# Kernel tuning notes

Hardware: AMD Instinct MI355X
Metric: run time of the kernel (lower is better)

## Reference

```python
import jax, jax.numpy as jnp
import numpy as np
from jax import lax

C = 173            # EEG channels (independent towers)
L = 400            # samples per channel
POOL_OUT = 10      # AdaptiveMaxPool1d output length (400/10 = 40 exact window)
EPS = 1e-5


def setup_inputs() -> dict:
    key = jax.random.key(0)
    ks = jax.random.split(key, 6)
    B = 64
    x = jax.random.normal(ks[0], (B, C, L), dtype=jnp.float32)
    # per-channel tower 1: Conv1d(1,16,9)  -> grouped kernel [C*16, 1, 9]
    w1 = jax.random.normal(ks[1], (C * 16, 1, 9), dtype=jnp.float32) * 0.2
    b1 = jnp.zeros((C * 16,), jnp.float32)
    g1 = jnp.ones((C * 16,), jnp.float32)
    beta1 = jnp.zeros((C * 16,), jnp.float32)
    m1 = jnp.zeros((C * 16,), jnp.float32)
    v1 = jnp.ones((C * 16,), jnp.float32)
    # per-channel tower 2: Conv1d(16,32,7) -> grouped kernel [C*32, 16, 7]
    w2 = jax.random.normal(ks[2], (C * 32, 16, 7), dtype=jnp.float32) * 0.05
    b2 = jnp.zeros((C * 32,), jnp.float32)
    g2 = jnp.ones((C * 32,), jnp.float32)
    beta2 = jnp.zeros((C * 32,), jnp.float32)
    m2 = jnp.zeros((C * 32,), jnp.float32)
    v2 = jnp.ones((C * 32,), jnp.float32)
    # combiner MLP: Linear(32*C*10, 128) -> ReLU -> Linear(128, 1)
    wc1 = jax.random.normal(ks[3], (128, 32 * C * POOL_OUT), dtype=jnp.float32) * 0.01
    bc1 = jnp.zeros((128,), jnp.float32)
    wc2 = jax.random.normal(ks[4], (1, 128), dtype=jnp.float32) * 0.05
    bc2 = jnp.zeros((1,), jnp.float32)
    return dict(x=x, w1=w1, b1=b1, g1=g1, beta1=beta1, m1=m1, v1=v1,
                w2=w2, b2=b2, g2=g2, beta2=beta2, m2=m2, v2=v2,
                wc1=wc1, bc1=bc1, wc2=wc2, bc2=bc2)


def _bn(y, g, beta, m, v):
    # inference-mode BatchNorm1d over channel axis of [B, CF, L]
    inv = g * lax.rsqrt(v + EPS)
    return y * inv[None, :, None] + (beta - m * inv)[None, :, None]


def reference(x, w1, b1, g1, beta1, m1, v1, w2, b2, g2, beta2, m2, v2, wc1, bc1, wc2, bc2):
    B = x.shape[0]
    dn = ('NCH', 'OIH', 'NCH')
    # tower conv 1: all 173 per-channel Conv1d(1,16,9,pad=4) as one grouped conv
    y = lax.conv_general_dilated(x, w1, (1,), [(4, 4)], dimension_numbers=dn,
                                 feature_group_count=C)           # [B, C*16, 400]
    y = jax.nn.relu(_bn(y + b1[None, :, None], g1, beta1, m1, v1))
    # tower conv 2: Conv1d(16,32,7,pad=3), grouped by channel
    y = lax.conv_general_dilated(y, w2, (1,), [(3, 3)], dimension_numbers=dn,
                                 feature_group_count=C)           # [B, C*32, 400]
    y = jax.nn.relu(_bn(y + b2[None, :, None], g2, beta2, m2, v2))
    # AdaptiveMaxPool1d(10): exact non-overlapping windows of 40
    y = y.reshape(B, C * 32, POOL_OUT, L // POOL_OUT).max(axis=-1)  # [B, C*32, 10]
    # concat of per-channel flattened features == flatten (channel, feat, pos)
    flat = y.reshape(B, C * 32 * POOL_OUT)                          # [B, 55360]
    h = jax.nn.relu(flat @ wc1.T + bc1)
    out = h @ wc2.T + bc2                                           # [B, 1]
    return out
```

## Files before the change

kernel.cpp:

```cpp
#include <hip/hip_runtime.h>

#define C_CH 173
#define L_IN 400
#define EPSV 1e-5f
#define KFEAT 55360

typedef __fp16   fp16x2 __attribute__((ext_vector_type(2)));
typedef _Float16 f16x8  __attribute__((ext_vector_type(8)));
typedef float    f32x4  __attribute__((ext_vector_type(4)));
typedef float    f32x16 __attribute__((ext_vector_type(16)));

#define Y1T_STRIDE_I 9
#define Y1T_ROWS   406

#define SEG_STRIDE 102

#define N1 (173 * 3584)
#define N2 (173 * 512)
#define N3 (173 * 96)

__global__ __launch_bounds__(256) void prep_kernel(
    const float* __restrict__ w1, const float* __restrict__ b1,
    const float* __restrict__ g1, const float* __restrict__ beta1,
    const float* __restrict__ m1, const float* __restrict__ v1,
    const float* __restrict__ w2, const float* __restrict__ b2,
    const float* __restrict__ g2, const float* __restrict__ beta2,
    const float* __restrict__ m2, const float* __restrict__ v2,
    _Float16* __restrict__ w2T_g, _Float16* __restrict__ w1T_g,
    float* __restrict__ sc_g)
{
    const int idx = blockIdx.x * 256 + threadIdx.x;
    if (idx < N1) {
        int c = idx / 3584, r = idx - c * 3584;
        int dt = r >> 9, fg = r & 511;
        int f = fg >> 4, g = fg & 15;
        w2T_g[idx] = (_Float16)w2[c * 3584 + f * 112 + g * 7 + dt];
    } else if (idx < N1 + N2) {
        int j = idx - N1;
        int c = j / 512, r = j - c * 512;
        int g = r >> 5, k = r & 31;
        w1T_g[j] = (k < 9) ? (_Float16)w1[c * 144 + g * 9 + k] : (_Float16)0.0f;
    } else if (idx < N1 + N2 + N3) {
        int j = idx - N1 - N2;
        int c = j / 96, r = j - c * 96;
        float o;
        if (r < 32) {
            int g  = r & 15;
            int cf = c * 16 + g;
            float inv = g1[cf] * rsqrtf(v1[cf] + EPSV);
            o = (r < 16) ? inv : (b1[cf] - m1[cf]) * inv + beta1[cf];
        } else {
            int f  = (r - 32) & 31;
            int cf = c * 32 + f;
            float inv = g2[cf] * rsqrtf(v2[cf] + EPSV);
            o = (r < 64) ? inv : (b2[cf] - m2[cf]) * inv + beta2[cf];
        }
        sc_g[j] = o;
    }
}

__global__ __launch_bounds__(320, 8) void tower_kernel(
    const float* __restrict__ x,
    const _Float16* __restrict__ w2T_g, const _Float16* __restrict__ w1T_g,
    const float* __restrict__ sc_g,
    _Float16* __restrict__ featH)
{
    __shared__ __align__(16) _Float16 xa_s[432];
    __shared__ __align__(16) _Float16 xb_s[432];
    __shared__ __align__(16) _Float16 w1T_s[16 * 32];
    __shared__ __align__(16) _Float16 y1T_s[Y1T_ROWS * 2 * Y1T_STRIDE_I];
    __shared__ __align__(16) _Float16 w2T_s[7 * 512];
    __shared__ _Float16               segmax_s[32 * SEG_STRIDE];
    __shared__ __align__(16) float    cst_s[96];

    const int c   = blockIdx.x;
    const int tid = threadIdx.x;

    {
        const int4* w2src = (const int4*)(w2T_g + (size_t)c * 3584);
        for (int i = tid; i < 448; i += 320) ((int4*)w2T_s)[i] = w2src[i];
        const int4* w1src = (const int4*)(w1T_g + c * 512);
        if (tid < 64) ((int4*)w1T_s)[tid] = w1src[tid];
        const float4* csrc = (const float4*)(sc_g + c * 96);
        if (tid >= 64 && tid < 88) ((float4*)cst_s)[tid - 64] = csrc[tid - 64];
        if (tid >= 88 && tid < 142) {
            int i = tid - 88;
            int r = i / 9, cx = i - r * 9;
            int row = (r < 3) ? r : (400 + r);
            ((int*)y1T_s)[row * Y1T_STRIDE_I + cx] = 0;
        }
    }
    __syncthreads();
    const float s2f  = cst_s[32 + (tid & 31)];
    const float sh2f = cst_s[64 + (tid & 31)];

    for (int nb = 0; nb < 4; ++nb) {
        const int b = blockIdx.y * 4 + nb;

        const float* xrow = x + ((size_t)b * C_CH + c) * L_IN;
        for (int i = tid; i < 432; i += 320) {
            float v = (i >= 4 && i < 404) ? xrow[i - 4] : 0.0f;
            _Float16 h = (_Float16)v;
            xa_s[i] = h;
            if (i > 0) xb_s[i - 1] = h;
        }
        if (tid == 0) xb_s[431] = (_Float16)0.0f;
        __syncthreads();

        {
            const int lane = tid & 63;
            const int wv5  = tid >> 6;
            const int nl   = lane & 15;
            const int q    = lane >> 4;
            union { int4 v; f16x8 h; } a1;
            a1.v = *(const int4*)((const int*)w1T_s + nl * 16 + q * 4);
            float s1r[4], sh1r[4];
#pragma unroll
            for (int r = 0; r < 4; ++r) {
                s1r[r]  = cst_s[q * 4 + r];
                sh1r[r] = cst_s[16 + q * 4 + r];
            }
            const int* xsel = (const int*)((nl & 1) ? xb_s : xa_s);
            for (int tile = 0; tile < 5; ++tile) {
                const int t0 = (wv5 * 5 + tile) * 16;
                const int dw = (t0 + nl + q * 8) >> 1;
                union { int4 v; f16x8 h; } bf;
                bf.v.x = xsel[dw];
                bf.v.y = xsel[dw + 1];
                bf.v.z = xsel[dw + 2];
                bf.v.w = xsel[dw + 3];
                f32x4 acc = {0.0f, 0.0f, 0.0f, 0.0f};
                acc = __builtin_amdgcn_mfma_f32_16x16x32_f16(a1.h, bf.h, acc, 0, 0, 0);
                union { _Float16 h[4]; int2 d; } pk;
#pragma unroll
                for (int r = 0; r < 4; ++r) {
                    float v = acc[r] * s1r[r] + sh1r[r];
                    pk.h[r] = (_Float16)(v > 0.0f ? v : 0.0f);
                }
                int* yp = (int*)y1T_s + (t0 + nl + 3) * Y1T_STRIDE_I + q * 2;
                yp[0] = pk.d.x;
                yp[1] = pk.d.y;
            }
        }
        __syncthreads();

        {
            const int wv    = tid >> 6;
            const int lane  = tid & 63;
            const int nlane = lane & 31;
            const int half  = lane >> 5;

            union F8q { int4 q; f16x8 h; } af[7];
#pragma unroll
            for (int dt = 0; dt < 7; ++dt)
                af[dt].q = *(const int4*)((const int*)w2T_s + dt * 256 + nlane * 8 + half * 4);

            for (int tile = wv; tile < 13; tile += 5) {
                const int tA  = tile * 32 + nlane;
                const int tAr = tA < 400 ? tA : 399;
                f32x16 acc;
#pragma unroll
                for (int i = 0; i < 16; ++i) acc[i] = 0.0f;

#pragma unroll
                for (int dt = 0; dt < 7; ++dt) {
                    const int* p = (const int*)y1T_s + (tAr + dt) * Y1T_STRIDE_I + half * 4;
                    union { int d[4]; f16x8 h; } bf;
                    bf.d[0] = p[0];
                    bf.d[1] = p[1];
                    bf.d[2] = p[2];
                    bf.d[3] = p[3];
                    acc = __builtin_amdgcn_mfma_f32_32x32x16_f16(bf.h, af[dt].h, acc, 0, 0, 0);
                }

                const int base = nlane * SEG_STRIDE + tile * 8 + half;
#pragma unroll
                for (int q = 0; q < 4; ++q) {
                    float v0 = acc[4 * q + 0] * s2f;
                    float v1 = acc[4 * q + 1] * s2f;
                    float v2 = acc[4 * q + 2] * s2f;
                    float v3 = acc[4 * q + 3] * s2f;
                    float m  = fmaxf(fmaxf(v0, v1), fmaxf(v2, v3));
                    const int sub = tile * 8 + 2 * q + half;
                    if (sub < 100) segmax_s[base + 2 * q] = (_Float16)m;
                }
            }
        }
        __syncthreads();

        {
            const int f = tid & 31;
            const int p = tid >> 5;
            float m = -3.0e38f;
#pragma unroll
            for (int k = 0; k < 10; ++k)
                m = fmaxf(m, (float)segmax_s[f * SEG_STRIDE + p * 10 + k]);
            float v = fmaxf(m + sh2f, 0.0f);
            featH[(size_t)b * KFEAT + (c * 32 + f) * 10 + p] = (_Float16)v;
        }
    }
}

__global__ __launch_bounds__(256) void fc1_kernel(
    const _Float16* __restrict__ featH, const float* __restrict__ wc1,
    float* __restrict__ part)
{
    const int tid   = threadIdx.x;
    const int kb    = blockIdx.x;
    const int k0    = kb * 320;
    const int lane  = tid & 63;
    const int wv    = tid >> 6;
    const int nlane = lane & 31;
    const int half  = lane >> 5;
    const int jrow  = wv * 32 + nlane;

    const float*    ap  = wc1   + (size_t)jrow * KFEAT + k0 + half * 8;
    const _Float16* b0p = featH + (size_t)nlane * KFEAT + k0 + half * 8;
    const _Float16* b1p = featH + (size_t)(nlane + 32) * KFEAT + k0 + half * 8;

    f32x16 acc0, acc1;
#pragma unroll
    for (int i = 0; i < 16; ++i) { acc0[i] = 0.0f; acc1[i] = 0.0f; }

#pragma unroll 2
    for (int s = 0; s < 20; ++s) {
        const float4 aw0 = *(const float4*)(ap + s * 16);
        const float4 aw1 = *(const float4*)(ap + s * 16 + 4);
        union { fp16x2 v2[4]; f16x8 h; } a;
        a.v2[0] = __builtin_amdgcn_cvt_pkrtz(aw0.x, aw0.y);
        a.v2[1] = __builtin_amdgcn_cvt_pkrtz(aw0.z, aw0.w);
        a.v2[2] = __builtin_amdgcn_cvt_pkrtz(aw1.x, aw1.y);
        a.v2[3] = __builtin_amdgcn_cvt_pkrtz(aw1.z, aw1.w);

        union { int4 q; f16x8 h; } b0, b1;
        b0.q = *(const int4*)(b0p + s * 16);
        b1.q = *(const int4*)(b1p + s * 16);

        acc0 = __builtin_amdgcn_mfma_f32_32x32x16_f16(a.h, b0.h, acc0, 0, 0, 0);
        acc1 = __builtin_amdgcn_mfma_f32_32x32x16_f16(a.h, b1.h, acc1, 0, 0, 0);
    }

    float* pt = part + (size_t)kb * 8192;
#pragma unroll
    for (int reg = 0; reg < 16; ++reg) {
        int j = wv * 32 + (reg & 3) + 8 * (reg >> 2) + 4 * half;
        pt[j * 64 + nlane]      = acc0[reg];
        pt[j * 64 + 32 + nlane] = acc1[reg];
    }
}

__global__ __launch_bounds__(256) void reduce_kernel(
    const float* __restrict__ part, float* __restrict__ h_ws)
{
    const int idx = blockIdx.x * 256 + threadIdx.x;
    float s = 0.0f;
    for (int kb = 0; kb < 173; ++kb)
        s += part[(size_t)kb * 8192 + idx];
    h_ws[idx] = s;
}

__global__ __launch_bounds__(64) void fc2_kernel(
    const float* __restrict__ h_ws, const float* __restrict__ bc1,
    const float* __restrict__ wc2, const float* __restrict__ bc2,
    float* __restrict__ out)
{
    const int b = threadIdx.x;
    float acc = bc2[0];
    for (int j = 0; j < 128; ++j) {
        float hv = h_ws[j * 64 + b] + bc1[j];
        hv = hv > 0.0f ? hv : 0.0f;
        acc += wc2[j] * hv;
    }
    out[b] = acc;
}

extern "C" void kernel_launch(void* const* d_in, const int* in_sizes, int n_in,
                              void* d_out, int out_size, void* d_ws, size_t ws_size,
                              hipStream_t stream)
{
    const float* x     = (const float*)d_in[0];
    const float* w1    = (const float*)d_in[1];
    const float* b1    = (const float*)d_in[2];
    const float* g1    = (const float*)d_in[3];
    const float* beta1 = (const float*)d_in[4];
    const float* m1    = (const float*)d_in[5];
    const float* v1    = (const float*)d_in[6];
    const float* w2    = (const float*)d_in[7];
    const float* b2    = (const float*)d_in[8];
    const float* g2    = (const float*)d_in[9];
    const float* beta2 = (const float*)d_in[10];
    const float* m2    = (const float*)d_in[11];
    const float* v2    = (const float*)d_in[12];
    const float* wc1   = (const float*)d_in[13];
    const float* bc1   = (const float*)d_in[14];
    const float* wc2   = (const float*)d_in[15];
    const float* bc2   = (const float*)d_in[16];

    char* ws = (char*)d_ws;
    _Float16* featH = (_Float16*)ws;
    float*    part  = (float*)(ws + 7086080);
    float*    h_ws  = (float*)(ws + 12754944);
    _Float16* w2T_g = (_Float16*)(ws + 12787712);
    _Float16* w1T_g = (_Float16*)(ws + 14027776);
    float*    sc_g  = (float*)(ws + 14204928);

    hipLaunchKernelGGL(prep_kernel, dim3(2834), dim3(256), 0, stream,
                       w1, b1, g1, beta1, m1, v1,
                       w2, b2, g2, beta2, m2, v2, w2T_g, w1T_g, sc_g);

    hipLaunchKernelGGL(tower_kernel, dim3(C_CH, 16), dim3(320), 0, stream,
                       x, w2T_g, w1T_g, sc_g, featH);

    hipLaunchKernelGGL(fc1_kernel, dim3(173), dim3(256), 0, stream,
                       featH, wc1, part);

    hipLaunchKernelGGL(reduce_kernel, dim3(32), dim3(256), 0, stream,
                       part, h_ws);

    hipLaunchKernelGGL(fc2_kernel, dim3(1), dim3(64), 0, stream,
                       h_ws, bc1, wc2, bc2, (float*)d_out);
}
```

Before: 209.3 us.

## Fuse fc1 split-K reduction via atomics, drop reduce kernel, slim tower LDS

The fc1 kernel now uses 512 threads, splitting each block's K range across two wave groups and combining them in shared memory, then atomically accumulating into a zero-initialized h buffer. This removes the partial-sum buffer and the separate reduce kernel launch. The tower kernel stops staging w1/w2 weights in LDS and reads them directly from global memory (w2 fragments per dt inside the tile loop), merges the two x buffers, and hoists the layer-1 setup out of the batch loop to cut LDS use and raise occupancy. fc2 is parallelised over 512 threads. Atomics make the summation order nondeterministic, and per-tile global weight loads may add latency.

```diff
diff --git a/kernel.cpp b/kernel.cpp
--- a/kernel.cpp
+++ b/kernel.cpp
@@ -15,9 +15,12 @@
 
 #define SEG_STRIDE 102
 
+#define XA_PAD 448
+
 #define N1 (173 * 3584)
 #define N2 (173 * 512)
 #define N3 (173 * 96)
+#define NH 8192
 
 __global__ __launch_bounds__(256) void prep_kernel(
     const float* __restrict__ w1, const float* __restrict__ b1,
@@ -27,7 +30,7 @@
     const float* __restrict__ g2, const float* __restrict__ beta2,
     const float* __restrict__ m2, const float* __restrict__ v2,
     _Float16* __restrict__ w2T_g, _Float16* __restrict__ w1T_g,
-    float* __restrict__ sc_g)
+    float* __restrict__ sc_g, float* __restrict__ h_ws)
 {
     const int idx = blockIdx.x * 256 + threadIdx.x;
     if (idx < N1) {
@@ -56,6 +59,8 @@
             o = (r < 64) ? inv : (b2[cf] - m2[cf]) * inv + beta2[cf];
         }
         sc_g[j] = o;
+    } else if (idx < N1 + N2 + N3 + NH) {
+        h_ws[idx - N1 - N2 - N3] = 0.0f;
     }
 }
 
@@ -65,11 +70,8 @@
     const float* __restrict__ sc_g,
     _Float16* __restrict__ featH)
 {
-    __shared__ __align__(16) _Float16 xa_s[432];
-    __shared__ __align__(16) _Float16 xb_s[432];
-    __shared__ __align__(16) _Float16 w1T_s[16 * 32];
+    __shared__ __align__(16) _Float16 xs_s[XA_PAD + 432];
     __shared__ __align__(16) _Float16 y1T_s[Y1T_ROWS * 2 * Y1T_STRIDE_I];
-    __shared__ __align__(16) _Float16 w2T_s[7 * 512];
     __shared__ _Float16               segmax_s[32 * SEG_STRIDE];
     __shared__ __align__(16) float    cst_s[96];
 
@@ -77,22 +79,35 @@
     const int tid = threadIdx.x;
 
     {
-        const int4* w2src = (const int4*)(w2T_g + (size_t)c * 3584);
-        for (int i = tid; i < 448; i += 320) ((int4*)w2T_s)[i] = w2src[i];
-        const int4* w1src = (const int4*)(w1T_g + c * 512);
-        if (tid < 64) ((int4*)w1T_s)[tid] = w1src[tid];
         const float4* csrc = (const float4*)(sc_g + c * 96);
-        if (tid >= 64 && tid < 88) ((float4*)cst_s)[tid - 64] = csrc[tid - 64];
-        if (tid >= 88 && tid < 142) {
-            int i = tid - 88;
+        if (tid < 24) ((float4*)cst_s)[tid] = csrc[tid];
+        if (tid >= 64 && tid < 118) {
+            int i = tid - 64;
             int r = i / 9, cx = i - r * 9;
             int row = (r < 3) ? r : (400 + r);
             ((int*)y1T_s)[row * Y1T_STRIDE_I + cx] = 0;
         }
     }
     __syncthreads();
-    const float s2f  = cst_s[32 + (tid & 31)];
-    const float sh2f = cst_s[64 + (tid & 31)];
+
+    const int lane  = tid & 63;
+    const int wv    = tid >> 6;
+    const int nlane = lane & 31;
+    const int half  = lane >> 5;
+    const float s2f  = cst_s[32 + nlane];
+    const float sh2f = cst_s[64 + nlane];
+
+    const int nl = lane & 15;
+    const int q1 = lane >> 4;
+    union { int4 v; f16x8 h; } a1;
+    a1.v = ((const int4*)(w1T_g + (size_t)c * 512))[nl * 4 + q1];
+    float s1r[4], sh1r[4];
+#pragma unroll
+    for (int r = 0; r < 4; ++r) {
+        s1r[r]  = cst_s[q1 * 4 + r];
+        sh1r[r] = cst_s[16 + q1 * 4 + r];
+    }
+    const int4* w2p = (const int4*)(w2T_g + (size_t)c * 3584);
 
     for (int nb = 0; nb < 4; ++nb) {
         const int b = blockIdx.y * 4 + nb;
@@ -101,29 +116,17 @@
         for (int i = tid; i < 432; i += 320) {
             float v = (i >= 4 && i < 404) ? xrow[i - 4] : 0.0f;
             _Float16 h = (_Float16)v;
-            xa_s[i] = h;
-            if (i > 0) xb_s[i - 1] = h;
-        }
-        if (tid == 0) xb_s[431] = (_Float16)0.0f;
+            xs_s[i] = h;
+            if (i > 0) xs_s[XA_PAD + i - 1] = h;
+        }
+        if (tid == 0) xs_s[XA_PAD + 431] = (_Float16)0.0f;
         __syncthreads();
 
         {
-            const int lane = tid & 63;
-            const int wv5  = tid >> 6;
-            const int nl   = lane & 15;
-            const int q    = lane >> 4;
-            union { int4 v; f16x8 h; } a1;
-            a1.v = *(const int4*)((const int*)w1T_s + nl * 16 + q * 4);
-            float s1r[4], sh1r[4];
-#pragma unroll
-            for (int r = 0; r < 4; ++r) {
-                s1r[r]  = cst_s[q * 4 + r];
-                sh1r[r] = cst_s[16 + q * 4 + r];
-            }
-            const int* xsel = (const int*)((nl & 1) ? xb_s : xa_s);
+            const int* xsel = (const int*)((nl & 1) ? (xs_s + XA_PAD) : xs_s);
             for (int tile = 0; tile < 5; ++tile) {
-                const int t0 = (wv5 * 5 + tile) * 16;
-                const int dw = (t0 + nl + q * 8) >> 1;
+                const int t0 = (wv * 5 + tile) * 16;
+                const int dw = (t0 + nl + q1 * 8) >> 1;
                 union { int4 v; f16x8 h; } bf;
                 bf.v.x = xsel[dw];
                 bf.v.y = xsel[dw + 1];
@@ -137,7 +140,7 @@
                     float v = acc[r] * s1r[r] + sh1r[r];
                     pk.h[r] = (_Float16)(v > 0.0f ? v : 0.0f);
                 }
-                int* yp = (int*)y1T_s + (t0 + nl + 3) * Y1T_STRIDE_I + q * 2;
+                int* yp = (int*)y1T_s + (t0 + nl + 3) * Y1T_STRIDE_I + q1 * 2;
                 yp[0] = pk.d.x;
                 yp[1] = pk.d.y;
             }
@@ -145,16 +148,6 @@
         __syncthreads();
 
         {
-            const int wv    = tid >> 6;
-            const int lane  = tid & 63;
-            const int nlane = lane & 31;
-            const int half  = lane >> 5;
-
-            union F8q { int4 q; f16x8 h; } af[7];
-#pragma unroll
-            for (int dt = 0; dt < 7; ++dt)
-                af[dt].q = *(const int4*)((const int*)w2T_s + dt * 256 + nlane * 8 + half * 4);
-
             for (int tile = wv; tile < 13; tile += 5) {
                 const int tA  = tile * 32 + nlane;
                 const int tAr = tA < 400 ? tA : 399;
@@ -164,13 +157,15 @@
 
 #pragma unroll
                 for (int dt = 0; dt < 7; ++dt) {
+                    union { int4 q; f16x8 h; } af;
+                    af.q = w2p[dt * 64 + nlane * 2 + half];
                     const int* p = (const int*)y1T_s + (tAr + dt) * Y1T_STRIDE_I + half * 4;
                     union { int d[4]; f16x8 h; } bf;
                     bf.d[0] = p[0];
                     bf.d[1] = p[1];
                     bf.d[2] = p[2];
                     bf.d[3] = p[3];
-                    acc = __builtin_amdgcn_mfma_f32_32x32x16_f16(bf.h, af[dt].h, acc, 0, 0, 0);
+                    acc = __builtin_amdgcn_mfma_f32_32x32x16_f16(bf.h, af.h, acc, 0, 0, 0);
                 }
 
                 const int base = nlane * SEG_STRIDE + tile * 8 + half;
@@ -201,18 +196,21 @@
     }
 }
 
-__global__ __launch_bounds__(256) void fc1_kernel(
+__global__ __launch_bounds__(512) void fc1_kernel(
     const _Float16* __restrict__ featH, const float* __restrict__ wc1,
-    float* __restrict__ part)
-{
+    float* __restrict__ h_ws)
+{
+    __shared__ float red[4 * 2048];
+
     const int tid   = threadIdx.x;
-    const int kb    = blockIdx.x;
-    const int k0    = kb * 320;
+    const int w     = tid >> 6;
     const int lane  = tid & 63;
-    const int wv    = tid >> 6;
     const int nlane = lane & 31;
     const int half  = lane >> 5;
-    const int jrow  = wv * 32 + nlane;
+    const int kh    = w >> 2;
+    const int jq    = w & 3;
+    const int jrow  = jq * 32 + nlane;
+    const int k0    = blockIdx.x * 320 + kh * 160;
 
     const float*    ap  = wc1   + (size_t)jrow * KFEAT + k0 + half * 8;
     const _Float16* b0p = featH + (size_t)nlane * KFEAT + k0 + half * 8;
@@ -222,8 +220,8 @@
 #pragma unroll
     for (int i = 0; i < 16; ++i) { acc0[i] = 0.0f; acc1[i] = 0.0f; }
 
-#pragma unroll 2
-    for (int s = 0; s < 20; ++s) {
+#pragma unroll 5
+    for (int s = 0; s < 10; ++s) {
         const float4 aw0 = *(const float4*)(ap + s * 16);
         const float4 aw1 = *(const float4*)(ap + s * 16 + 4);
         union { fp16x2 v2[4]; f16x8 h; } a;
@@ -240,38 +238,53 @@
         acc1 = __builtin_amdgcn_mfma_f32_32x32x16_f16(a.h, b1.h, acc1, 0, 0, 0);
     }
 
-    float* pt = part + (size_t)kb * 8192;
-#pragma unroll
-    for (int reg = 0; reg < 16; ++reg) {
-        int j = wv * 32 + (reg & 3) + 8 * (reg >> 2) + 4 * half;
-        pt[j * 64 + nlane]      = acc0[reg];
-        pt[j * 64 + 32 + nlane] = acc1[reg];
-    }
-}
-
-__global__ __launch_bounds__(256) void reduce_kernel(
-    const float* __restrict__ part, float* __restrict__ h_ws)
-{
-    const int idx = blockIdx.x * 256 + threadIdx.x;
-    float s = 0.0f;
-    for (int kb = 0; kb < 173; ++kb)
-        s += part[(size_t)kb * 8192 + idx];
-    h_ws[idx] = s;
-}
-
-__global__ __launch_bounds__(64) void fc2_kernel(
+    if (kh == 1) {
+        float* rp = red + jq * 2048;
+#pragma unroll
+        for (int reg = 0; reg < 16; ++reg) {
+            rp[(reg * 2 + half) * 64 + nlane]      = acc0[reg];
+            rp[(reg * 2 + half) * 64 + 32 + nlane] = acc1[reg];
+        }
+    }
+    __syncthreads();
+    if (kh == 0) {
+        const float* rp = red + jq * 2048;
+#pragma unroll
+        for (int reg = 0; reg < 16; ++reg) {
+            int j = jq * 32 + (reg & 3) + 8 * (reg >> 2) + 4 * half;
+            float v0 = acc0[reg] + rp[(reg * 2 + half) * 64 + nlane];
+            float v1 = acc1[reg] + rp[(reg * 2 + half) * 64 + 32 + nlane];
+            atomicAdd(&h_ws[j * 64 + nlane], v0);
+            atomicAdd(&h_ws[j * 64 + 32 + nlane], v1);
+        }
+    }
+}
+
+__global__ __launch_bounds__(512) void fc2_kernel(
     const float* __restrict__ h_ws, const float* __restrict__ bc1,
     const float* __restrict__ wc2, const float* __restrict__ bc2,
     float* __restrict__ out)
 {
-    const int b = threadIdx.x;
-    float acc = bc2[0];
-    for (int j = 0; j < 128; ++j) {
+    __shared__ float partial[512];
+    const int t  = threadIdx.x;
+    const int b  = t & 63;
+    const int jc = t >> 6;
+    float s = 0.0f;
+#pragma unroll
+    for (int jj = 0; jj < 16; ++jj) {
+        const int j = jc * 16 + jj;
         float hv = h_ws[j * 64 + b] + bc1[j];
         hv = hv > 0.0f ? hv : 0.0f;
-        acc += wc2[j] * hv;
-    }
-    out[b] = acc;
+        s += wc2[j] * hv;
+    }
+    partial[t] = s;
+    __syncthreads();
+    if (t < 64) {
+        float r = partial[t];
+#pragma unroll
+        for (int k = 1; k < 8; ++k) r += partial[t + 64 * k];
+        out[b] = r + bc2[0];
+    }
 }
 
 extern "C" void kernel_launch(void* const* d_in, const int* in_sizes, int n_in,
@@ -298,25 +311,21 @@
 
     char* ws = (char*)d_ws;
     _Float16* featH = (_Float16*)ws;
-    float*    part  = (float*)(ws + 7086080);
-    float*    h_ws  = (float*)(ws + 12754944);
-    _Float16* w2T_g = (_Float16*)(ws + 12787712);
-    _Float16* w1T_g = (_Float16*)(ws + 14027776);
-    float*    sc_g  = (float*)(ws + 14204928);
-
-    hipLaunchKernelGGL(prep_kernel, dim3(2834), dim3(256), 0, stream,
+    _Float16* w2T_g = (_Float16*)(ws + 7086080);
+    _Float16* w1T_g = (_Float16*)(ws + 8326144);
+    float*    sc_g  = (float*)(ws + 8503296);
+    float*    h_ws  = (float*)(ws + 8569728);
+
+    hipLaunchKernelGGL(prep_kernel, dim3(2865), dim3(256), 0, stream,
                        w1, b1, g1, beta1, m1, v1,
-                       w2, b2, g2, beta2, m2, v2, w2T_g, w1T_g, sc_g);
+                       w2, b2, g2, beta2, m2, v2, w2T_g, w1T_g, sc_g, h_ws);
 
     hipLaunchKernelGGL(tower_kernel, dim3(C_CH, 16), dim3(320), 0, stream,
                        x, w2T_g, w1T_g, sc_g, featH);
 
-    hipLaunchKernelGGL(fc1_kernel, dim3(173), dim3(256), 0, stream,
-                       featH, wc1, part);
-
-    hipLaunchKernelGGL(reduce_kernel, dim3(32), dim3(256), 0, stream,
-                       part, h_ws);
-
-    hipLaunchKernelGGL(fc2_kernel, dim3(1), dim3(64), 0, stream,
+    hipLaunchKernelGGL(fc1_kernel, dim3(173), dim3(512), 0, stream,
+                       featH, wc1, h_ws);
+
+    hipLaunchKernelGGL(fc2_kernel, dim3(1), dim3(512), 0, stream,
                        h_ws, bc1, wc2, bc2, (float*)d_out);
 }
```

Measured after the change: 265.4 us. 26.8% more time.
